# Kernel optimization log

Hardware: AMD Instinct MI355X
Metric: run time of the kernel (lower is better)

Reference implementation:

```python
import jax, jax.numpy as jnp
import numpy as np

NUM_HEADS = 8
ALPHA = 4.0
KSIZE = 5


def _pow_relu(x, p):
    # relu(x) ** p, safe for x<=0 (avoids 0**p grad NaNs wrt p)
    pos = x > 0
    xs = jnp.where(pos, x, 1.0)
    return jnp.where(pos, xs ** p, 0.0)


def setup_inputs() -> dict:
    key = jax.random.key(0)
    ks = jax.random.split(key, 10)
    B, N, C = 16, 3136, 512
    hd = C // NUM_HEADS
    s = 0.02
    return {
        "x": jax.random.normal(ks[0], (B, N, C), jnp.float32),
        "qg_w": jax.random.normal(ks[1], (C, 2 * C), jnp.float32) * s,
        "kv_w": jax.random.normal(ks[2], (C, 2 * C), jnp.float32) * s,
        "proj_w": jax.random.normal(ks[3], (C, C), jnp.float32) * s,
        "proj_b": jax.random.normal(ks[4], (C,), jnp.float32) * s,
        "pos_enc": jax.random.normal(ks[5], (1, N, C), jnp.float32) * s,
        "scale_p": jax.random.normal(ks[6], (1, 1, C), jnp.float32) * s,
        "power_p": jax.random.normal(ks[7], (1, NUM_HEADS, 1, hd), jnp.float32) * s,
        "dwc_w": jax.random.normal(ks[8], (hd, 1, KSIZE, KSIZE), jnp.float32) * s,
        "dwc_b": jax.random.normal(ks[9], (hd,), jnp.float32) * s,
        "H": 56,
        "W": 56,
    }


def _forward(x, qg_w, kv_w, proj_w, proj_b, pos_enc, scale_p, power_p, dwc_w, dwc_b, H, W):
    B, N, C = x.shape
    nh = NUM_HEADS
    hd = C // nh
    n = N  # sr_ratio == 1

    qg = x @ qg_w                      # [B,N,2C]
    q, g = qg[..., :C], qg[..., C:]
    kv = x @ kv_w                      # [B,N,2C]
    k, v = kv[..., :C], kv[..., C:]
    k = k + pos_enc

    scale = jax.nn.softplus(scale_p)   # [1,1,C]
    q = q / scale
    k = k / scale

    def heads(t):  # [B,N,C] -> [B,nh,N,hd]
        return t.reshape(B, -1, nh, hd).transpose(0, 2, 1, 3)

    q, k, v = heads(q), heads(k), heads(v)

    power = 1.0 + ALPHA * jax.nn.sigmoid(power_p)  # [1,nh,1,hd]
    q_pos = _pow_relu(q, power)
    q_neg = _pow_relu(-q, power)
    q_sim = jnp.concatenate([q_pos, q_neg], -1)    # [B,nh,N,2hd]
    q_opp = jnp.concatenate([q_neg, q_pos], -1)
    kf = jnp.concatenate([_pow_relu(k, power), _pow_relu(-k, power)], -1)  # [B,nh,n,2hd]

    v1, v2 = kf.shape[-1] // 4, None  # v chunks below
    v1, v2 = jnp.split(v, 2, axis=-1)               # each [B,nh,n,hd/2]

    km = kf.mean(axis=2)                            # [B,nh,2hd]
    inv_n = 1.0 / n

    def branch(qf, vv):
        z = 1.0 / (jnp.einsum('bhnd,bhd->bhn', qf, km) + 1e-6)
        kv_ = jnp.einsum('bhnd,bhne->bhde', kf, vv) * inv_n   # (n^-0.5)*(n^-0.5)
        return jnp.einsum('bhnd,bhde->bhne', qf, kv_) * z[..., None]

    x_sim = branch(q_sim, v1)
    x_opp = branch(q_opp, v2)
    xo = jnp.concatenate([x_sim, x_opp], -1)        # [B,nh,N,hd]
    xo = xo.transpose(0, 2, 1, 3).reshape(B, N, C)

    # depthwise conv residual on v
    vimg = v.reshape(B * nh, H, W, hd).transpose(0, 3, 1, 2)  # [B*nh,hd,H,W]
    pad = KSIZE // 2
    vd = jax.lax.conv_general_dilated(
        vimg, dwc_w, window_strides=(1, 1), padding=((pad, pad), (pad, pad)),
        feature_group_count=hd) + dwc_b[None, :, None, None]
    vd = vd.reshape(B, C, N).transpose(0, 2, 1)     # [B,N,C]

    out = (xo + vd) * g
    return out @ proj_w + proj_b


def reference(x, qg_w, kv_w, proj_w, proj_b, pos_enc, scale_p, power_p, dwc_w, dwc_b, H, W):
    return _forward(x, qg_w, kv_w, proj_w, proj_b, pos_enc, scale_p, power_p, dwc_w, dwc_b, H, W)
```

## Files before the change

### kernel.cpp

```cpp
#include <hip/hip_runtime.h>
#include <math.h>

typedef unsigned short ushort;
typedef __attribute__((ext_vector_type(8))) short short8v;
typedef __attribute__((ext_vector_type(4))) short short4v;
typedef __attribute__((ext_vector_type(4))) float float4v;
typedef __attribute__((ext_vector_type(8))) __bf16 bf16x8;

#define NHEADS 8
#define NPOS 3136
#define MROWS 50176
#define KDIM 512

__device__ __forceinline__ ushort f2bf(float f) {
  union { float f; unsigned u; } x; x.f = f;
  unsigned r = x.u + 0x7fffu + ((x.u >> 16) & 1u);
  return (ushort)(r >> 16);
}
__device__ __forceinline__ float bf2f(ushort h) {
  union { unsigned u; float f; } x; x.u = ((unsigned)h) << 16; return x.f;
}

__device__ __forceinline__ float4v mfma16(short8v a, short8v b, float4v c) {
  return __builtin_amdgcn_mfma_f32_16x16x32_bf16(
      __builtin_bit_cast(bf16x8, a), __builtin_bit_cast(bf16x8, b), c, 0, 0, 0);
}

__device__ __forceinline__ void glds16(const void* g, void* l) {
  __builtin_amdgcn_global_load_lds(
      (const __attribute__((address_space(1))) unsigned int*)g,
      (__attribute__((address_space(3))) unsigned int*)l, 16, 0, 0);
}

__device__ __forceinline__ float fexp2(float x) {
  float r; asm("v_exp_f32 %0, %1" : "=v"(r) : "v"(x)); return r;
}
__device__ __forceinline__ float flog2(float x) {
  float r; asm("v_log_f32 %0, %1" : "=v"(r) : "v"(x)); return r;
}

__global__ __launch_bounds__(512) void prep_kernel(const float* __restrict__ scale_p,
                                                   const float* __restrict__ power_p,
                                                   float* __restrict__ scinv,
                                                   float* __restrict__ pwr)
{
  int t = threadIdx.x;
  if (t < KDIM) {
    scinv[t] = 1.f / log1pf(expf(scale_p[t]));
    pwr[t]   = 1.f + 4.f / (1.f + expf(-power_p[t]));
  }
}

__global__ __launch_bounds__(256) void cvt_x_kernel(const float* __restrict__ x,
                                                    ushort* __restrict__ xb)
{
  const size_t i = ((size_t)blockIdx.x * 256 + threadIdx.x) * 4;
  float4v v = *(const float4v*)(x + i);
  short4v o = { (short)f2bf(v[0]), (short)f2bf(v[1]), (short)f2bf(v[2]), (short)f2bf(v[3]) };
  *(short4v*)(xb + i) = o;
}

__global__ __launch_bounds__(256) void transpose_w_kernel(const float* __restrict__ src,
                                                          ushort* __restrict__ dst,
                                                          int K, int N)
{
  __shared__ float tile[32][33];
  const int t = threadIdx.x, tx = t & 31, ty = t >> 5;
  const int nb = blockIdx.x * 32, kb = blockIdx.y * 32;
  #pragma unroll
  for (int i = 0; i < 4; i++)
    tile[ty + i*8][tx] = src[(size_t)(kb + ty + i*8) * N + nb + tx];
  __syncthreads();
  #pragma unroll
  for (int i = 0; i < 4; i++)
    dst[(size_t)(nb + ty + i*8) * K + kb + tx] = f2bf(tile[tx][ty + i*8]);
}

__global__ __launch_bounds__(512, 6) void gemm_bf16_kernel(
    const ushort* __restrict__ A, const ushort* __restrict__ Bt, int mode,
    const float* __restrict__ scinv, const float* __restrict__ pwr,
    const float* __restrict__ pos_enc, const float* __restrict__ bias,
    float* __restrict__ outf, ushort* __restrict__ outb0, ushort* __restrict__ outb1,
    int nbx_shift)
{
  __shared__ ushort As[3][128*32];
  __shared__ ushort Bs[3][128*32];
  const int t = threadIdx.x;
  const int wave = t >> 6, lane = t & 63;

  const int nwg = (int)(gridDim.x * gridDim.y);
  const int lid = (int)(blockIdx.y * gridDim.x + blockIdx.x);
  const int nlid = (lid & 7) * (nwg >> 3) + (lid >> 3);
  const int bx = nlid & ((1 << nbx_shift) - 1);
  const int by = nlid >> nbx_shift;
  const int m0 = by * 128, n0 = bx * 128;

  const int wm = wave >> 2, wn = wave & 3;
  const int lm = lane & 15, q = lane >> 4;

  const int srow = t >> 2;
  const int lc = ((t & 3) ^ (srow & 3) ^ ((srow >> 2) & 3)) * 8;
  const ushort* gA = A  + (size_t)(m0 + srow) * KDIM + lc;
  const ushort* gB = Bt + (size_t)(n0 + srow) * KDIM + lc;

  const int pc = (q ^ (lm & 3) ^ ((lm >> 2) & 3)) * 8;
  const int arow = wm * 64 + lm;
  const int brow = wn * 32 + lm;

  float4v acc[4][2];
  #pragma unroll
  for (int i = 0; i < 4; i++)
    #pragma unroll
    for (int j = 0; j < 2; j++) { float4v z = {0.f,0.f,0.f,0.f}; acc[i][j] = z; }

  glds16(gA,      &As[0][t*8]);
  glds16(gB,      &Bs[0][t*8]);
  glds16(gA + 32, &As[1][t*8]);
  glds16(gB + 32, &Bs[1][t*8]);

  #pragma unroll
  for (int kt = 0; kt < 16; kt++) {
    if (kt < 15) asm volatile("s_waitcnt vmcnt(2)" ::: "memory");
    else         asm volatile("s_waitcnt vmcnt(0)" ::: "memory");
    __builtin_amdgcn_sched_barrier(0);
    __builtin_amdgcn_s_barrier();
    if (kt + 2 < 16) {
      const int nb = (kt + 2) % 3;
      glds16(gA + (kt + 2) * 32, &As[nb][t*8]);
      glds16(gB + (kt + 2) * 32, &Bs[nb][t*8]);
    }
    const int cb = kt % 3;
    short8v a[4], b[2];
    #pragma unroll
    for (int i = 0; i < 4; i++)
      a[i] = *(const short8v*)&As[cb][(arow + i*16) * 32 + pc];
    #pragma unroll
    for (int j = 0; j < 2; j++)
      b[j] = *(const short8v*)&Bs[cb][(brow + j*16) * 32 + pc];
    #pragma unroll
    for (int i = 0; i < 4; i++)
      #pragma unroll
      for (int j = 0; j < 2; j++)
        acc[i][j] = mfma16(a[i], b[j], acc[i][j]);
  }

  const int rq = (lane >> 4) * 4;
  #pragma unroll
  for (int i = 0; i < 4; i++) {
    #pragma unroll
    for (int r = 0; r < 4; r++) {
      const int grow = m0 + wm * 64 + i * 16 + rq + r;
      const int bb = grow / NPOS;
      const int nn = grow - bb * NPOS;
      #pragma unroll
      for (int j = 0; j < 2; j++) {
        const int gcol = n0 + wn * 32 + j * 16 + lm;
        const float val = acc[i][j][r];
        if (mode == 2) {
          outf[(size_t)grow * 512 + gcol] = val + bias[gcol];
        } else if (gcol < 512) {
          float sv;
          if (mode == 0) sv = val * scinv[gcol];
          else           sv = (val + pos_enc[(size_t)nn * 512 + gcol]) * scinv[gcol];
          const float pw = pwr[gcol];
          const float aq = fabsf(sv);
          const float f = fexp2(pw * flog2(aq));
          const unsigned fb = (unsigned)f2bf(f);
          unsigned pack = 0;
          if (sv > 0.f)      pack = fb;
          else if (sv < 0.f) pack = fb << 16;
          const int h = gcol >> 6, d = gcol & 63;
          unsigned* qrow = (unsigned*)(outb0 + (((size_t)((bb << 3) + h) * NPOS + nn) << 7));
          qrow[d] = pack;
        } else {
          const int c2 = gcol - 512;
          if (mode == 0) {
            outb1[(size_t)grow * 512 + c2] = f2bf(val);
          } else {
            const int h = c2 >> 6, d = c2 & 63;
            outb1[(((size_t)((bb << 3) + h) * NPOS + nn) << 6) + d] = f2bf(val);
          }
        }
      }
    }
  }
}

#define RSPLIT 8
#define RCHUNK 392
__global__ __launch_bounds__(256) void reduce_kv_kernel(
    const ushort* __restrict__ KF, const ushort* __restrict__ Vb,
    float* __restrict__ pkv, float* __restrict__ pkm)
{
  const int bh = blockIdx.x >> 3, s = blockIdx.x & 7;
  const int t = threadIdx.x;
  __shared__ ushort kf_s[8*128];
  __shared__ ushort v_s[8*64];
  const int td = t & 31, te = t >> 5;
  const int d4 = td * 4, e8 = te * 8;
  float acc[4][8];
  #pragma unroll
  for (int c = 0; c < 4; c++)
    #pragma unroll
    for (int e = 0; e < 8; e++) acc[c][e] = 0.f;
  float km4[4] = {0.f,0.f,0.f,0.f};
  const int nbase = s * RCHUNK;

  for (int g = 0; g < RCHUNK/8; g++) {
    const int n = nbase + g*8;
    *(short4v*)&kf_s[(t>>5)*128 + (t&31)*4] =
        *(const short4v*)&KF[(((size_t)bh*NPOS + n + (t>>5)) << 7) + (t&31)*4];
    if (t < 128)
      *(short4v*)&v_s[(t>>4)*64 + (t&15)*4] =
          *(const short4v*)&Vb[(((size_t)bh*NPOS + n + (t>>4)) << 6) + (t&15)*4];
    __syncthreads();
    #pragma unroll
    for (int i = 0; i < 8; i++) {
      short4v k4 = *(const short4v*)&kf_s[i*128 + d4];
      short8v v8 = *(const short8v*)&v_s[i*64 + e8];
      float kf4[4], vf[8];
      #pragma unroll
      for (int c = 0; c < 4; c++) kf4[c] = bf2f((ushort)k4[c]);
      #pragma unroll
      for (int e = 0; e < 8; e++) vf[e] = bf2f((ushort)v8[e]);
      if (te == 0) {
        #pragma unroll
        for (int c = 0; c < 4; c++) km4[c] += kf4[c];
      }
      #pragma unroll
      for (int c = 0; c < 4; c++)
        #pragma unroll
        for (int e = 0; e < 8; e++) acc[c][e] = fmaf(kf4[c], vf[e], acc[c][e]);
    }
    __syncthreads();
  }
  float* op = pkv + ((size_t)(s*128 + bh) << 13);
  #pragma unroll
  for (int c = 0; c < 4; c++) {
    float4v o0 = {acc[c][0], acc[c][1], acc[c][2], acc[c][3]};
    float4v o1 = {acc[c][4], acc[c][5], acc[c][6], acc[c][7]};
    *(float4v*)&op[(d4+c)*64 + e8]     = o0;
    *(float4v*)&op[(d4+c)*64 + e8 + 4] = o1;
  }
  if (te == 0) {
    #pragma unroll
    for (int c = 0; c < 4; c++) pkm[((size_t)(s*128 + bh) << 7) + d4 + c] = km4[c];
  }
}

__global__ __launch_bounds__(256) void reduce_final_kernel(
    const float* __restrict__ pkv, const float* __restrict__ pkm,
    ushort* __restrict__ Kt)
{
  const int bh = blockIdx.x, t = threadIdx.x;
  const float inv_n = 1.f / (float)NPOS;
  for (int i = t; i < 8192; i += 256) {
    float s = 0.f;
    #pragma unroll
    for (int sp = 0; sp < RSPLIT; sp++) s += pkv[((size_t)(sp*128 + bh) << 13) + i];
    const int d = i >> 6, e = i & 63;
    const int dd = (e < 32) ? d : (d ^ 1);
    Kt[((size_t)bh*80 + e)*128 + dd] = f2bf(s * inv_n);
  }
  if (t < 128) {
    float s = 0.f;
    #pragma unroll
    for (int sp = 0; sp < RSPLIT; sp++) s += pkm[((size_t)(sp*128 + bh) << 7) + t];
    const ushort b = f2bf(s * inv_n);
    Kt[((size_t)bh*80 + 64)*128 + t] = b;
    Kt[((size_t)bh*80 + 65)*128 + (t ^ 1)] = b;
  }
  for (int i = t; i < 14*128; i += 256) Kt[((size_t)bh*80 + 66)*128 + i] = 0;
}

__global__ __launch_bounds__(256) void attn_mfma_kernel(
    const ushort* __restrict__ QS, const ushort* __restrict__ Kt,
    ushort* __restrict__ XO)
{
  __shared__ ushort qs_s[128*128];
  __shared__ ushort kv_s[80*128];
  const int t = threadIdx.x, wave = t >> 6, lane = t & 63;
  const int bh = blockIdx.y;
  const int n0 = blockIdx.x * 128;

  const ushort* ksrc = Kt + (size_t)bh * 80 * 128;
  #pragma unroll
  for (int j = 0; j < 5; j++) {
    const int elem = (j*4096 + wave*1024) >> 1;
    glds16(ksrc + elem + lane*8, kv_s + elem);
  }
  const ushort* qsrc = QS + ((size_t)bh * NPOS + n0) * 128;
  #pragma unroll
  for (int j = 0; j < 8; j++) {
    const int elem = (j*4096 + wave*1024) >> 1;
    glds16(qsrc + elem + lane*8, qs_s + elem);
  }
  __syncthreads();

  const int lm = lane & 15, q8 = (lane >> 4) * 8;
  float4v acc[2][5];
  #pragma unroll
  for (int i = 0; i < 2; i++)
    #pragma unroll
    for (int j = 0; j < 5; j++) { float4v z = {0.f,0.f,0.f,0.f}; acc[i][j] = z; }

  #pragma unroll
  for (int ks = 0; ks < 4; ks++) {
    short8v a[2], b[5];
    #pragma unroll
    for (int i = 0; i < 2; i++)
      a[i] = *(const short8v*)&qs_s[(wave*32 + i*16 + lm)*128 + ks*32 + q8];
    #pragma unroll
    for (int j = 0; j < 5; j++)
      b[j] = *(const short8v*)&kv_s[(j*16 + lm)*128 + ks*32 + q8];
    #pragma unroll
    for (int i = 0; i < 2; i++)
      #pragma unroll
      for (int j = 0; j < 5; j++)
        acc[i][j] = mfma16(a[i], b[j], acc[i][j]);
  }

  const int rq = (lane >> 4) * 4;
  #pragma unroll
  for (int i = 0; i < 2; i++) {
    #pragma unroll
    for (int r = 0; r < 4; r++) {
      const int n = n0 + wave*32 + i*16 + rq + r;
      const float dsim = __shfl(acc[i][4][r], lane & 48);
      const float dopp = __shfl(acc[i][4][r], (lane & 48) | 1);
      const float zs = 1.f / (dsim + 1e-6f);
      const float zo = 1.f / (dopp + 1e-6f);
      if (n < NPOS) {
        ushort* orow = XO + (((size_t)bh * NPOS + n) << 6);
        #pragma unroll
        for (int j = 0; j < 4; j++)
          orow[j*16 + lm] = f2bf(acc[i][j][r] * ((j < 2) ? zs : zo));
      }
    }
  }
}

__global__ __launch_bounds__(256) void conv_combine_kernel(
    const ushort* __restrict__ Vb, const ushort* __restrict__ XO,
    const ushort* __restrict__ g, const float* __restrict__ dwc_w,
    const float* __restrict__ dwc_b, ushort* __restrict__ cmb)
{
  __shared__ ushort vs[6*60*64];
  const int t = threadIdx.x;
  const int bh = blockIdx.y, b = bh >> 3, h = bh & 7;
  const int y0 = blockIdx.x * 2;
  for (int i = t; i < 5760; i += 256) {
    const int ry = i / 960;
    const int rem = i - ry * 960;
    const int xx = (rem >> 4) - 2;
    const int c4 = (rem & 15) * 4;
    const int yy = y0 - 2 + ry;
    short4v val = {0,0,0,0};
    if (yy >= 0 && yy < 56 && xx >= 0 && xx < 56)
      val = *(const short4v*)&Vb[(((size_t)bh*NPOS + yy*56 + xx) << 6) + c4];
    *(short4v*)&vs[ry*3840 + (rem >> 4)*64 + c4] = val;
  }
  __syncthreads();

  const int c = t & 63, xg = t >> 6;
  float w[25];
  #pragma unroll
  for (int i = 0; i < 25; i++) w[i] = dwc_w[c*25 + i];
  const float bias = dwc_b[c];

  #pragma unroll
  for (int y = 0; y < 2; y++) {
    float acc[14];
    #pragma unroll
    for (int xi = 0; xi < 14; xi++) acc[xi] = bias;
    #pragma unroll
    for (int ky = 0; ky < 5; ky++) {
      const ushort* row = &vs[(y + ky)*3840 + (xg*14)*64 + c];
      #pragma unroll
      for (int xl = 0; xl < 18; xl++) {
        const float val = bf2f(row[xl*64]);
        #pragma unroll
        for (int kx = 0; kx < 5; kx++) {
          const int xi = xl - kx;
          if (xi >= 0 && xi < 14)
            acc[xi] = fmaf(w[ky*5 + kx], val, acc[xi]);
        }
      }
    }
    const int yo = y0 + y;
    #pragma unroll
    for (int xi = 0; xi < 14; xi++) {
      const int n = yo*56 + xg*14 + xi;
      const float xov = bf2f(XO[(((size_t)bh*NPOS + n) << 6) + c]);
      const size_t nat = ((size_t)b*NPOS + n)*512 + h*64 + c;
      cmb[nat] = f2bf((xov + acc[xi]) * bf2f(g[nat]));
    }
  }
}

extern "C" void kernel_launch(void* const* d_in, const int* in_sizes, int n_in,
                              void* d_out, int out_size, void* d_ws, size_t ws_size,
                              hipStream_t stream)
{
  const float* x       = (const float*)d_in[0];
  const float* qg_w    = (const float*)d_in[1];
  const float* kv_w    = (const float*)d_in[2];
  const float* proj_w  = (const float*)d_in[3];
  const float* proj_b  = (const float*)d_in[4];
  const float* pos_enc = (const float*)d_in[5];
  const float* scale_p = (const float*)d_in[6];
  const float* power_p = (const float*)d_in[7];
  const float* dwc_w   = (const float*)d_in[8];
  const float* dwc_b   = (const float*)d_in[9];
  float* out = (float*)d_out;

  const size_t MCs = (size_t)MROWS * 512;
  ushort* xbf = (ushort*)d_ws;
  ushort* KQ  = xbf + MCs;
  ushort* Vb  = KQ + 2*MCs + 8192;
  ushort* Kt  = Vb + MCs;
  ushort* wqg = Kt + (size_t)128*80*128;
  ushort* wkv = wqg + (size_t)1024*512;
  ushort* wpj = wkv + (size_t)1024*512;
  float* pkv  = (float*)(wpj + (size_t)512*512);
  float* pkm  = pkv + (size_t)RSPLIT*128*8192;
  float* scinv= pkm + (size_t)RSPLIT*128*128;
  float* pwr  = scinv + 512;
  const size_t need = (size_t)((char*)(pwr + 512) - (char*)d_ws);
  if (ws_size < need) return;

  ushort* XOb = xbf;
  ushort* cmb = KQ;
  ushort* gbuf = (ushort*)out;

  prep_kernel<<<1, 512, 0, stream>>>(scale_p, power_p, scinv, pwr);
  cvt_x_kernel<<<(int)(MCs/4/256), 256, 0, stream>>>(x, xbf);
  transpose_w_kernel<<<dim3(32,16), 256, 0, stream>>>(qg_w,   wqg, 512, 1024);
  transpose_w_kernel<<<dim3(32,16), 256, 0, stream>>>(kv_w,   wkv, 512, 1024);
  transpose_w_kernel<<<dim3(16,16), 256, 0, stream>>>(proj_w, wpj, 512, 512);

  gemm_bf16_kernel<<<dim3(8, MROWS/128), 512, 0, stream>>>(
      xbf, wkv, 1, scinv, pwr, pos_enc, nullptr, nullptr, KQ, Vb, 3);
  reduce_kv_kernel<<<128*RSPLIT, 256, 0, stream>>>(KQ, Vb, pkv, pkm);
  reduce_final_kernel<<<128, 256, 0, stream>>>(pkv, pkm, Kt);
  gemm_bf16_kernel<<<dim3(8, MROWS/128), 512, 0, stream>>>(
      xbf, wqg, 0, scinv, pwr, nullptr, nullptr, nullptr, KQ, gbuf, 3);
  attn_mfma_kernel<<<dim3(25, 128), 256, 0, stream>>>(KQ, Kt, XOb);
  conv_combine_kernel<<<dim3(28, 128), 256, 0, stream>>>(Vb, XOb, gbuf, dwc_w, dwc_b, cmb);
  gemm_bf16_kernel<<<dim3(4, MROWS/128), 512, 0, stream>>>(
      cmb, wpj, 2, nullptr, nullptr, nullptr, proj_b, out, nullptr, nullptr, 2);
}
```

Baseline: 751.3 us.

## Transpose KV GEMM output to feature-major and use MFMA for KV reduction

The KV projection GEMM now computes the transposed product (weights times x), so K features and V come out feature-major with positions contiguous, and pos_enc is pre-transposed into scratch space in the output buffer. The KV reduction becomes an MFMA GEMM over position chunks, with 7 splits, and the K mean comes from an extra MFMA against a ones vector. The goal is to replace the scalar FMA reduction with matrix-core work. The depthwise conv staging is rewritten to read the new V layout into a padded shared tile. The cost is strided scalar 2-byte stores in the GEMM epilogue and per-element gathers in the conv load, and it relies on the output buffer as scratch for peT.

```diff
diff --git a/kernel.cpp b/kernel.cpp
--- a/kernel.cpp
+++ b/kernel.cpp
@@ -74,6 +74,21 @@
   #pragma unroll
   for (int i = 0; i < 4; i++)
     dst[(size_t)(nb + ty + i*8) * K + kb + tx] = f2bf(tile[tx][ty + i*8]);
+}
+
+__global__ __launch_bounds__(256) void transpose_pe_kernel(const float* __restrict__ src,
+                                                           float* __restrict__ dst)
+{
+  __shared__ float tile[32][33];
+  const int t = threadIdx.x, tx = t & 31, ty = t >> 5;
+  const int nb = blockIdx.x * 32, kb = blockIdx.y * 32;
+  #pragma unroll
+  for (int i = 0; i < 4; i++)
+    tile[ty + i*8][tx] = src[(size_t)(kb + ty + i*8) * 512 + nb + tx];
+  __syncthreads();
+  #pragma unroll
+  for (int i = 0; i < 4; i++)
+    dst[(size_t)(nb + ty + i*8) * NPOS + kb + tx] = tile[tx][ty + i*8];
 }
 
 __global__ __launch_bounds__(512, 6) void gemm_bf16_kernel(
@@ -93,7 +108,8 @@
   const int nlid = (lid & 7) * (nwg >> 3) + (lid >> 3);
   const int bx = nlid & ((1 << nbx_shift) - 1);
   const int by = nlid >> nbx_shift;
-  const int m0 = by * 128, n0 = bx * 128;
+  const int m0 = ((mode == 3) ? bx : by) * 128;
+  const int n0 = ((mode == 3) ? by : bx) * 128;
 
   const int wm = wave >> 2, wn = wave & 3;
   const int lm = lane & 15, q = lane >> 4;
@@ -145,106 +161,164 @@
   }
 
   const int rq = (lane >> 4) * 4;
-  #pragma unroll
-  for (int i = 0; i < 4; i++) {
-    #pragma unroll
-    for (int r = 0; r < 4; r++) {
-      const int grow = m0 + wm * 64 + i * 16 + rq + r;
-      const int bb = grow / NPOS;
-      const int nn = grow - bb * NPOS;
+  if (mode == 3) {
+    #pragma unroll
+    for (int i = 0; i < 4; i++) {
+      const int of0 = m0 + wm * 64 + i * 16 + rq;
       #pragma unroll
       for (int j = 0; j < 2; j++) {
-        const int gcol = n0 + wn * 32 + j * 16 + lm;
-        const float val = acc[i][j][r];
-        if (mode == 2) {
-          outf[(size_t)grow * 512 + gcol] = val + bias[gcol];
-        } else if (gcol < 512) {
-          float sv;
-          if (mode == 0) sv = val * scinv[gcol];
-          else           sv = (val + pos_enc[(size_t)nn * 512 + gcol]) * scinv[gcol];
-          const float pw = pwr[gcol];
-          const float aq = fabsf(sv);
-          const float f = fexp2(pw * flog2(aq));
-          const unsigned fb = (unsigned)f2bf(f);
-          unsigned pack = 0;
-          if (sv > 0.f)      pack = fb;
-          else if (sv < 0.f) pack = fb << 16;
-          const int h = gcol >> 6, d = gcol & 63;
-          unsigned* qrow = (unsigned*)(outb0 + (((size_t)((bb << 3) + h) * NPOS + nn) << 7));
-          qrow[d] = pack;
-        } else {
-          const int c2 = gcol - 512;
-          if (mode == 0) {
-            outb1[(size_t)grow * 512 + c2] = f2bf(val);
+        const int gn = n0 + wn * 32 + j * 16;
+        const int bb = gn / NPOS;
+        const int nn = gn - bb * NPOS + lm;
+        #pragma unroll
+        for (int r = 0; r < 4; r++) {
+          const int o = of0 + r;
+          const float val = acc[i][j][r];
+          if (o < 512) {
+            const int h = o >> 6, d = o & 63;
+            const float sv = (val + pos_enc[(size_t)o * NPOS + nn]) * scinv[o];
+            const float pw = pwr[o];
+            const float aq = fabsf(sv);
+            const float f = fexp2(pw * flog2(aq));
+            const ushort fb = f2bf(f);
+            ushort* kr = outb0 + ((size_t)((bb << 3) + h) * 128 + 2 * d) * NPOS + nn;
+            kr[0]    = (sv > 0.f) ? fb : (ushort)0;
+            kr[NPOS] = (sv < 0.f) ? fb : (ushort)0;
           } else {
-            const int h = c2 >> 6, d = c2 & 63;
-            outb1[(((size_t)((bb << 3) + h) * NPOS + nn) << 6) + d] = f2bf(val);
+            const int ov = o - 512;
+            const int h = ov >> 6, e = ov & 63;
+            outb1[((size_t)((bb << 3) + h) * 64 + e) * NPOS + nn] = f2bf(val);
           }
         }
       }
     }
-  }
-}
-
-#define RSPLIT 8
-#define RCHUNK 392
-__global__ __launch_bounds__(256) void reduce_kv_kernel(
-    const ushort* __restrict__ KF, const ushort* __restrict__ Vb,
+  } else {
+    #pragma unroll
+    for (int i = 0; i < 4; i++) {
+      #pragma unroll
+      for (int r = 0; r < 4; r++) {
+        const int grow = m0 + wm * 64 + i * 16 + rq + r;
+        const int bb = grow / NPOS;
+        const int nn = grow - bb * NPOS;
+        #pragma unroll
+        for (int j = 0; j < 2; j++) {
+          const int gcol = n0 + wn * 32 + j * 16 + lm;
+          const float val = acc[i][j][r];
+          if (mode == 2) {
+            outf[(size_t)grow * 512 + gcol] = val + bias[gcol];
+          } else if (gcol < 512) {
+            const float sv = val * scinv[gcol];
+            const float pw = pwr[gcol];
+            const float aq = fabsf(sv);
+            const float f = fexp2(pw * flog2(aq));
+            const unsigned fb = (unsigned)f2bf(f);
+            unsigned pack = 0;
+            if (sv > 0.f)      pack = fb;
+            else if (sv < 0.f) pack = fb << 16;
+            const int h = gcol >> 6, d = gcol & 63;
+            unsigned* qrow = (unsigned*)(outb0 + (((size_t)((bb << 3) + h) * NPOS + nn) << 7));
+            qrow[d] = pack;
+          } else {
+            const int c2 = gcol - 512;
+            outb1[(size_t)grow * 512 + c2] = f2bf(val);
+          }
+        }
+      }
+    }
+  }
+}
+
+#define RSPLIT 7
+#define RK 448
+__global__ __launch_bounds__(256, 4) void reduce_kv_kernel(
+    const ushort* __restrict__ KFt, const ushort* __restrict__ Vt,
     float* __restrict__ pkv, float* __restrict__ pkm)
 {
-  const int bh = blockIdx.x >> 3, s = blockIdx.x & 7;
+  __shared__ ushort As[3][128*32];
+  __shared__ ushort Bs[3][64*32];
+  const int sp = blockIdx.x, bh = blockIdx.y;
   const int t = threadIdx.x;
-  __shared__ ushort kf_s[8*128];
-  __shared__ ushort v_s[8*64];
-  const int td = t & 31, te = t >> 5;
-  const int d4 = td * 4, e8 = te * 8;
-  float acc[4][8];
-  #pragma unroll
-  for (int c = 0; c < 4; c++)
-    #pragma unroll
-    for (int e = 0; e < 8; e++) acc[c][e] = 0.f;
-  float km4[4] = {0.f,0.f,0.f,0.f};
-  const int nbase = s * RCHUNK;
-
-  for (int g = 0; g < RCHUNK/8; g++) {
-    const int n = nbase + g*8;
-    *(short4v*)&kf_s[(t>>5)*128 + (t&31)*4] =
-        *(const short4v*)&KF[(((size_t)bh*NPOS + n + (t>>5)) << 7) + (t&31)*4];
-    if (t < 128)
-      *(short4v*)&v_s[(t>>4)*64 + (t&15)*4] =
-          *(const short4v*)&Vb[(((size_t)bh*NPOS + n + (t>>4)) << 6) + (t&15)*4];
-    __syncthreads();
-    #pragma unroll
-    for (int i = 0; i < 8; i++) {
-      short4v k4 = *(const short4v*)&kf_s[i*128 + d4];
-      short8v v8 = *(const short8v*)&v_s[i*64 + e8];
-      float kf4[4], vf[8];
-      #pragma unroll
-      for (int c = 0; c < 4; c++) kf4[c] = bf2f((ushort)k4[c]);
-      #pragma unroll
-      for (int e = 0; e < 8; e++) vf[e] = bf2f((ushort)v8[e]);
-      if (te == 0) {
-        #pragma unroll
-        for (int c = 0; c < 4; c++) km4[c] += kf4[c];
-      }
-      #pragma unroll
-      for (int c = 0; c < 4; c++)
-        #pragma unroll
-        for (int e = 0; e < 8; e++) acc[c][e] = fmaf(kf4[c], vf[e], acc[c][e]);
-    }
-    __syncthreads();
-  }
-  float* op = pkv + ((size_t)(s*128 + bh) << 13);
-  #pragma unroll
-  for (int c = 0; c < 4; c++) {
-    float4v o0 = {acc[c][0], acc[c][1], acc[c][2], acc[c][3]};
-    float4v o1 = {acc[c][4], acc[c][5], acc[c][6], acc[c][7]};
-    *(float4v*)&op[(d4+c)*64 + e8]     = o0;
-    *(float4v*)&op[(d4+c)*64 + e8 + 4] = o1;
-  }
-  if (te == 0) {
-    #pragma unroll
-    for (int c = 0; c < 4; c++) pkm[((size_t)(s*128 + bh) << 7) + d4 + c] = km4[c];
+  const int wave = t >> 6, lane = t & 63;
+  const int wm = wave >> 1, wn = wave & 1;
+  const int lm = lane & 15, q = lane >> 4;
+
+  const int r0 = t >> 2;
+  const int lc = ((t & 3) ^ (r0 & 3) ^ ((r0 >> 2) & 3)) * 8;
+  const ushort* gA = KFt + ((size_t)bh * 128 + r0) * NPOS + sp * RK + lc;
+  const ushort* gB = Vt  + ((size_t)bh * 64  + r0) * NPOS + sp * RK + lc;
+  const size_t A64 = (size_t)64 * NPOS;
+
+  const int pc = (q ^ (lm & 3) ^ ((lm >> 2) & 3)) * 8;
+  const int arow = wm * 64 + lm;
+  const int brow = wn * 32 + lm;
+
+  float4v acc[4][2], accK[4];
+  #pragma unroll
+  for (int i = 0; i < 4; i++) {
+    #pragma unroll
+    for (int j = 0; j < 2; j++) { float4v z = {0.f,0.f,0.f,0.f}; acc[i][j] = z; }
+    float4v z = {0.f,0.f,0.f,0.f}; accK[i] = z;
+  }
+  short8v bk;
+  #pragma unroll
+  for (int c = 0; c < 8; c++) bk[c] = (short)((lm == 0) ? 0x3F80 : 0);
+
+  glds16(gA,            &As[0][t*8]);
+  glds16(gA + A64,      &As[0][2048 + t*8]);
+  glds16(gB,            &Bs[0][t*8]);
+  glds16(gA + 32,       &As[1][t*8]);
+  glds16(gA + A64 + 32, &As[1][2048 + t*8]);
+  glds16(gB + 32,       &Bs[1][t*8]);
+
+  #pragma unroll
+  for (int kt = 0; kt < 14; kt++) {
+    if (kt < 13) asm volatile("s_waitcnt vmcnt(3)" ::: "memory");
+    else         asm volatile("s_waitcnt vmcnt(0)" ::: "memory");
+    __builtin_amdgcn_sched_barrier(0);
+    __builtin_amdgcn_s_barrier();
+    if (kt + 2 < 14) {
+      const int nb = (kt + 2) % 3;
+      const int off = (kt + 2) * 32;
+      glds16(gA + off,       &As[nb][t*8]);
+      glds16(gA + A64 + off, &As[nb][2048 + t*8]);
+      glds16(gB + off,       &Bs[nb][t*8]);
+    }
+    const int cb = kt % 3;
+    short8v a[4], b[2];
+    #pragma unroll
+    for (int i = 0; i < 4; i++)
+      a[i] = *(const short8v*)&As[cb][(arow + i*16) * 32 + pc];
+    #pragma unroll
+    for (int j = 0; j < 2; j++)
+      b[j] = *(const short8v*)&Bs[cb][(brow + j*16) * 32 + pc];
+    #pragma unroll
+    for (int i = 0; i < 4; i++)
+      #pragma unroll
+      for (int j = 0; j < 2; j++)
+        acc[i][j] = mfma16(a[i], b[j], acc[i][j]);
+    if (wn == 0) {
+      #pragma unroll
+      for (int i = 0; i < 4; i++)
+        accK[i] = mfma16(a[i], bk, accK[i]);
+    }
+  }
+
+  const int rq = q * 4;
+  float* op = pkv + (((size_t)sp * 128 + bh) << 13);
+  #pragma unroll
+  for (int i = 0; i < 4; i++)
+    #pragma unroll
+    for (int j = 0; j < 2; j++)
+      #pragma unroll
+      for (int r = 0; r < 4; r++)
+        op[(size_t)(wm*64 + i*16 + rq + r) * 64 + wn*32 + j*16 + lm] = acc[i][j][r];
+  if (wn == 0 && lm == 0) {
+    float* kp = pkm + (((size_t)sp * 128 + bh) << 7);
+    #pragma unroll
+    for (int i = 0; i < 4; i++)
+      #pragma unroll
+      for (int r = 0; r < 4; r++)
+        kp[wm*64 + i*16 + rq + r] = accK[i][r];
   }
 }
 
@@ -341,24 +415,25 @@
 }
 
 __global__ __launch_bounds__(256) void conv_combine_kernel(
-    const ushort* __restrict__ Vb, const ushort* __restrict__ XO,
+    const ushort* __restrict__ Vt, const ushort* __restrict__ XO,
     const ushort* __restrict__ g, const float* __restrict__ dwc_w,
     const float* __restrict__ dwc_b, ushort* __restrict__ cmb)
 {
-  __shared__ ushort vs[6*60*64];
+  __shared__ ushort vs[360*66];
   const int t = threadIdx.x;
   const int bh = blockIdx.y, b = bh >> 3, h = bh & 7;
   const int y0 = blockIdx.x * 2;
-  for (int i = t; i < 5760; i += 256) {
-    const int ry = i / 960;
-    const int rem = i - ry * 960;
-    const int xx = (rem >> 4) - 2;
-    const int c4 = (rem & 15) * 4;
-    const int yy = y0 - 2 + ry;
-    short4v val = {0,0,0,0};
-    if (yy >= 0 && yy < 56 && xx >= 0 && xx < 56)
-      val = *(const short4v*)&Vb[(((size_t)bh*NPOS + yy*56 + xx) << 6) + c4];
-    *(short4v*)&vs[ry*3840 + (rem >> 4)*64 + c4] = val;
+  for (int i = t; i < 24576; i += 256) {
+    const int xs = i & 63;
+    const int seg = i >> 6;
+    const int c = seg & 63, ry = seg >> 6;
+    if (xs < 60) {
+      const int yy = y0 - 2 + ry, xx = xs - 2;
+      ushort val = 0;
+      if (yy >= 0 && yy < 56 && xx >= 0 && xx < 56)
+        val = Vt[((size_t)bh*64 + c)*NPOS + yy*56 + xx];
+      vs[(ry*60 + xs)*66 + c] = val;
+    }
   }
   __syncthreads();
 
@@ -375,10 +450,10 @@
     for (int xi = 0; xi < 14; xi++) acc[xi] = bias;
     #pragma unroll
     for (int ky = 0; ky < 5; ky++) {
-      const ushort* row = &vs[(y + ky)*3840 + (xg*14)*64 + c];
+      const ushort* row = &vs[((y + ky)*60 + xg*14)*66 + c];
       #pragma unroll
       for (int xl = 0; xl < 18; xl++) {
-        const float val = bf2f(row[xl*64]);
+        const float val = bf2f(row[xl*66]);
         #pragma unroll
         for (int kx = 0; kx < 5; kx++) {
           const int xi = xl - kx;
@@ -417,8 +492,8 @@
   const size_t MCs = (size_t)MROWS * 512;
   ushort* xbf = (ushort*)d_ws;
   ushort* KQ  = xbf + MCs;
-  ushort* Vb  = KQ + 2*MCs + 8192;
-  ushort* Kt  = Vb + MCs;
+  ushort* Vt  = KQ + 2*MCs + 8192;
+  ushort* Kt  = Vt + MCs;
   ushort* wqg = Kt + (size_t)128*80*128;
   ushort* wkv = wqg + (size_t)1024*512;
   ushort* wpj = wkv + (size_t)1024*512;
@@ -432,21 +507,23 @@
   ushort* XOb = xbf;
   ushort* cmb = KQ;
   ushort* gbuf = (ushort*)out;
+  float* peT = (float*)d_out + 13000000;
 
   prep_kernel<<<1, 512, 0, stream>>>(scale_p, power_p, scinv, pwr);
   cvt_x_kernel<<<(int)(MCs/4/256), 256, 0, stream>>>(x, xbf);
   transpose_w_kernel<<<dim3(32,16), 256, 0, stream>>>(qg_w,   wqg, 512, 1024);
   transpose_w_kernel<<<dim3(32,16), 256, 0, stream>>>(kv_w,   wkv, 512, 1024);
   transpose_w_kernel<<<dim3(16,16), 256, 0, stream>>>(proj_w, wpj, 512, 512);
+  transpose_pe_kernel<<<dim3(16,98), 256, 0, stream>>>(pos_enc, peT);
 
   gemm_bf16_kernel<<<dim3(8, MROWS/128), 512, 0, stream>>>(
-      xbf, wkv, 1, scinv, pwr, pos_enc, nullptr, nullptr, KQ, Vb, 3);
-  reduce_kv_kernel<<<128*RSPLIT, 256, 0, stream>>>(KQ, Vb, pkv, pkm);
+      wkv, xbf, 3, scinv, pwr, peT, nullptr, nullptr, KQ, Vt, 3);
+  reduce_kv_kernel<<<dim3(RSPLIT, 128), 256, 0, stream>>>(KQ, Vt, pkv, pkm);
   reduce_final_kernel<<<128, 256, 0, stream>>>(pkv, pkm, Kt);
   gemm_bf16_kernel<<<dim3(8, MROWS/128), 512, 0, stream>>>(
       xbf, wqg, 0, scinv, pwr, nullptr, nullptr, nullptr, KQ, gbuf, 3);
   attn_mfma_kernel<<<dim3(25, 128), 256, 0, stream>>>(KQ, Kt, XOb);
-  conv_combine_kernel<<<dim3(28, 128), 256, 0, stream>>>(Vb, XOb, gbuf, dwc_w, dwc_b, cmb);
+  conv_combine_kernel<<<dim3(28, 128), 256, 0, stream>>>(Vt, XOb, gbuf, dwc_w, dwc_b, cmb);
   gemm_bf16_kernel<<<dim3(4, MROWS/128), 512, 0, stream>>>(
       cmb, wpj, 2, nullptr, nullptr, nullptr, proj_b, out, nullptr, nullptr, 2);
 }
```

Measured after the change: 757.4 us. About the same (+0.8%).
